# Optimization experiments

Hardware: AMD Instinct MI355X
Metric: run time of the kernel (lower is better)

## Reference

```python
import jax, jax.numpy as jnp
import numpy as np

DIM = 1024
N_HEADS = 16
HEAD_DIM = DIM // N_HEADS
B, T = 2, 2048


def setup_inputs() -> dict:
    key = jax.random.key(0)
    ks = jax.random.split(key, 5)
    x = jax.random.normal(ks[0], (B, T, DIM), dtype=jnp.float32)
    s = DIM ** -0.5
    Wq = jax.random.normal(ks[1], (DIM, DIM), dtype=jnp.float32) * s
    Wk = jax.random.normal(ks[2], (DIM, DIM), dtype=jnp.float32) * s
    Wv = jax.random.normal(ks[3], (DIM, DIM), dtype=jnp.float32) * s
    Wo = jax.random.normal(ks[4], (DIM, DIM), dtype=jnp.float32) * s
    # causal mask: 1 where attendable, 0 where masked (masked_fill on mask==0)
    mask = jnp.tril(jnp.ones((T, T), dtype=jnp.int32))[None, None, :, :]
    return {"x": x, "Wq": Wq, "Wk": Wk, "Wv": Wv, "Wo": Wo, "mask": mask}


def _rope_tables(seq_len, dim, dtype):
    inv_freq = 1.0 / (10000.0 ** (jnp.arange(0, dim, 2, dtype=jnp.float32) / dim))
    t = jnp.arange(seq_len, dtype=jnp.float32)
    freqs = jnp.outer(t, inv_freq)               # [T, dim/2]
    emb = jnp.concatenate([freqs, freqs], -1)    # [T, dim]
    return jnp.cos(emb).astype(dtype), jnp.sin(emb).astype(dtype)


def _rotate_half(t):
    h = t.shape[-1] // 2
    return jnp.concatenate([-t[..., h:], t[..., :h]], axis=-1)


def reference(x, Wq, Wk, Wv, Wo, mask):
    Bq, Tq, C = x.shape
    H, Dh = N_HEADS, C // N_HEADS
    q = (x @ Wq.T).reshape(Bq, Tq, H, Dh)
    k = (x @ Wk.T).reshape(Bq, Tq, H, Dh)
    v = (x @ Wv.T).reshape(Bq, Tq, H, Dh)
    cos, sin = _rope_tables(Tq, Dh, x.dtype)
    cos = cos[None, :, None, :]   # [1,T,1,Dh]
    sin = sin[None, :, None, :]
    q = q * cos + _rotate_half(q) * sin
    k = k * cos + _rotate_half(k) * sin
    scale = Dh ** -0.5
    # [B,H,T,T]
    attn = jnp.einsum('bqhd,bkhd->bhqk', q, k) * scale
    attn = jnp.where(mask == 0, jnp.float32(-jnp.inf).astype(attn.dtype), attn)
    attn = jax.nn.softmax(attn, axis=-1)
    out = jnp.einsum('bhqk,bkhd->bqhd', attn, v).reshape(Bq, Tq, C)
    return out @ Wo.T
```

## Files before the change

### kernel.cpp

```cpp
#include <hip/hip_runtime.h>
#include <stdint.h>


typedef float  f32x4  __attribute__((ext_vector_type(4)));
typedef float  f32x16 __attribute__((ext_vector_type(16)));
typedef __bf16 bf16x8 __attribute__((ext_vector_type(8)));
typedef unsigned int u32x2 __attribute__((ext_vector_type(2)));

#define GLDS16(gp, lp)                                                         \
  __builtin_amdgcn_global_load_lds(                                            \
      (const __attribute__((address_space(1))) void*)(gp),                     \
      (__attribute__((address_space(3))) void*)(lp), 16, 0, 0)

static __device__ __forceinline__ f32x4 zero4() {
  f32x4 z = {0.f, 0.f, 0.f, 0.f};
  return z;
}

static __device__ __forceinline__ bf16x8 cvt8(const float* __restrict__ p) {
  f32x4 u = *(const f32x4*)p;
  f32x4 v = *(const f32x4*)(p + 4);
  bf16x8 o;
#pragma unroll
  for (int j = 0; j < 4; ++j) o[j] = (__bf16)u[j];
#pragma unroll
  for (int j = 0; j < 4; ++j) o[4 + j] = (__bf16)v[j];
  return o;
}

__global__ __launch_bounds__(256) void prep(
    const float* __restrict__ x,
    const float* __restrict__ Wq, const float* __restrict__ Wk,
    const float* __restrict__ Wv, const float* __restrict__ Wo,
    __bf16* __restrict__ xb, __bf16* __restrict__ Wb)
{
  size_t g = ((size_t)blockIdx.x * 256 + threadIdx.x) * 8;
  if (g < (size_t)4194304) {
    *(bf16x8*)&xb[g] = cvt8(x + g);
  } else {
    size_t j = g - 4194304;
    int w = (int)(j >> 20);
    size_t off = j & 1048575;
    const float* src = (w == 0) ? Wq : (w == 1) ? Wk : (w == 2) ? Wv : Wo;
    *(bf16x8*)&Wb[(size_t)w * 1048576 + off] = cvt8(src + off);
  }
}

__global__ __launch_bounds__(256) void gemm_qkv(
    const __bf16* __restrict__ xb, const __bf16* __restrict__ Wb,
    __bf16* __restrict__ Qp, __bf16* __restrict__ Kp, __bf16* __restrict__ Vt)
{
  __shared__ __bf16 Smem[2][2 * 128 * 32];

  const int tid  = threadIdx.x;
  const int lane = tid & 63;
  const int wid  = tid >> 6;
  const int quad = lane >> 4;
  const int l16  = lane & 15;
  const int wm   = (wid >> 1) * 64;
  const int wn   = (wid & 1) * 64;

  const int lin = blockIdx.x;
  const int n0  = (lin & 7) * 128;
  const int r2  = lin >> 3;
  const int z   = r2 % 3;
  const int m0  = (r2 / 3) * 128;
  const __bf16* Bt = Wb + (size_t)z * 1048576;

  const int r0 = tid >> 2, c0 = tid & 3;
  const int r1 = r0 + 64;
  const int scx = (c0 ^ ((r0 >> 1) & 3)) * 8;
  const int fq  = (l16 >> 1) & 3;

  f32x4 acc[4][4];
  for (int i = 0; i < 4; ++i)
    for (int j = 0; j < 4; ++j) acc[i][j] = zero4();

#define QKV_STAGE(buf, k0)                                                     \
  do {                                                                         \
    __bf16* As_ = Smem[buf];                                                   \
    __bf16* Bs_ = Smem[buf] + 128 * 32;                                        \
    GLDS16(xb + (size_t)(m0 + r0) * 1024 + (k0) + scx, &As_[(size_t)tid * 8]); \
    GLDS16(xb + (size_t)(m0 + r1) * 1024 + (k0) + scx,                         \
           &As_[(size_t)(tid + 256) * 8]);                                     \
    GLDS16(Bt + (size_t)(n0 + r0) * 1024 + (k0) + scx, &Bs_[(size_t)tid * 8]); \
    GLDS16(Bt + (size_t)(n0 + r1) * 1024 + (k0) + scx,                         \
           &Bs_[(size_t)(tid + 256) * 8]);                                     \
  } while (0)

  QKV_STAGE(0, 0);
  __syncthreads();

  for (int k = 0; k < 32; ++k) {
    const int cur = k & 1;
    if (k < 31) QKV_STAGE(cur ^ 1, (k + 1) * 32);

    const __bf16* As = Smem[cur];
    const __bf16* Bs = Smem[cur] + 128 * 32;
    bf16x8 af[4], bfr[4];
#pragma unroll
    for (int i = 0; i < 4; ++i)
      af[i] = *(const bf16x8*)
          &As[(wm + i * 16 + l16) * 32 + ((quad ^ fq) * 8)];
#pragma unroll
    for (int i = 0; i < 4; ++i)
      bfr[i] = *(const bf16x8*)
          &Bs[(wn + i * 16 + l16) * 32 + ((quad ^ fq) * 8)];
    __builtin_amdgcn_s_setprio(1);
#pragma unroll
    for (int mt = 0; mt < 4; ++mt)
#pragma unroll
      for (int nt = 0; nt < 4; ++nt)
        acc[mt][nt] = __builtin_amdgcn_mfma_f32_16x16x32_bf16(
            af[mt], bfr[nt], acc[mt][nt], 0, 0, 0);
    __builtin_amdgcn_s_setprio(0);

    __syncthreads();
  }
#undef QKV_STAGE

  const int h = (n0 + wn) >> 6;
  __bf16* es = &Smem[0][wid * 1152];
  const int rl = lane >> 3, ch = lane & 7;

  if (z < 2) {
    const float c0f = -13.287712379549449f / 32.0f;
    const float f0 = exp2f((float)l16 * c0f);
    const float f1 = exp2f((float)(16 + l16) * c0f);
    const float SC = (z == 0) ? 0.125f * 1.44269504088896340736f : 1.0f;
    for (int mt = 0; mt < 4; ++mt)
      for (int r = 0; r < 4; ++r) {
        int gm = m0 + wm + mt * 16 + 4 * quad + r;
        float tt = (float)(gm & 2047);
        for (int nt = 0; nt < 2; ++nt) {
          float ang = tt * (nt ? f1 : f0);
          float cv = __cosf(ang) * SC, sv = __sinf(ang) * SC;
          float lo = acc[mt][nt][r], hi = acc[mt][nt + 2][r];
          acc[mt][nt][r]     = lo * cv - hi * sv;
          acc[mt][nt + 2][r] = hi * cv + lo * sv;
        }
      }
    __bf16* dst = (z == 0) ? Qp : Kp;
    for (int mt = 0; mt < 4; ++mt) {
      for (int nt = 0; nt < 4; ++nt)
        for (int r = 0; r < 4; ++r)
          es[(4 * quad + r) * 72 + nt * 16 + l16] = (__bf16)acc[mt][nt][r];
      size_t g0 = (size_t)(m0 + wm + mt * 16 + rl) * 1024 + n0 + wn + ch * 8;
      *(bf16x8*)&dst[g0]            = *(const bf16x8*)&es[rl * 72 + ch * 8];
      *(bf16x8*)&dst[g0 + 8 * 1024] = *(const bf16x8*)&es[(rl + 8) * 72 + ch * 8];
    }
  } else {
    const int b = m0 >> 11;
    const size_t hb = (size_t)(b * 16 + h) * 64;
    const int tt = (m0 + wm) & 2047;
    for (int nt = 0; nt < 4; ++nt) {
      for (int mt = 0; mt < 4; ++mt)
        for (int r = 0; r < 4; ++r)
          es[l16 * 72 + mt * 16 + 4 * quad + r] = (__bf16)acc[mt][nt][r];
      size_t g0 = (hb + nt * 16 + rl) * 2048 + tt + ch * 8;
      *(bf16x8*)&Vt[g0]                     = *(const bf16x8*)&es[rl * 72 + ch * 8];
      *(bf16x8*)&Vt[g0 + (size_t)8 * 2048]  = *(const bf16x8*)&es[(rl + 8) * 72 + ch * 8];
    }
  }
}

__global__ __launch_bounds__(256) void attn_fwd(
    __bf16* QA, const __bf16* __restrict__ Kp,
    const __bf16* __restrict__ Vt)
{
  __shared__ __bf16 Ks[2][64 * 64];
  __shared__ __bf16 Vs[2][64 * 64];

  const int tid  = threadIdx.x;
  const int lane = tid & 63, wid = tid >> 6;
  const int hl = lane >> 5, lq = lane & 31, lq7 = lq & 7;
  const int qh = wid & 1, kh = wid >> 1;

  const int L  = blockIdx.x;
  const int j  = L >> 3;
  const int qb = 31 - (j >> 2);
  const int bh = (L & 7) * 4 + (j & 3);
  const int b = bh >> 4, h = bh & 15;
  const int q0 = qb * 64;

  const size_t rowb = (size_t)b * 2048;
  const __bf16* Vb = Vt + (size_t)bh * 64 * 2048;

  const int srow = lane >> 3;
  const int scol = ((lane & 7) ^ srow) * 8;
  const int ck0 = wid * 2, ck1 = wid * 2 + 1;

  const int iql = qh * 32 + lq;

  bf16x8 qa[4];
#pragma unroll
  for (int ks = 0; ks < 4; ++ks)
    qa[ks] = *(const bf16x8*)
        &QA[(rowb + q0 + iql) * 1024 + h * 64 + ks * 16 + hl * 8];

  f32x16 oacc[2];
#pragma unroll
  for (int dt = 0; dt < 2; ++dt)
#pragma unroll
    for (int r = 0; r < 16; ++r) oacc[dt][r] = 0.f;
  float l_i = 0.f;

  const int kcmax = qb;

  GLDS16(Kp + (rowb + ck0 * 8 + srow) * 1024 + h * 64 + scol, &Ks[0][ck0 * 512]);
  GLDS16(Kp + (rowb + ck1 * 8 + srow) * 1024 + h * 64 + scol, &Ks[0][ck1 * 512]);
  GLDS16(Vb + (size_t)(ck0 * 8 + srow) * 2048 + scol, &Vs[0][ck0 * 512]);
  GLDS16(Vb + (size_t)(ck1 * 8 + srow) * 2048 + scol, &Vs[0][ck1 * 512]);
  __syncthreads();

  for (int kc = 0; kc <= kcmax; ++kc) {
    const int c = kc & 1;
    if (kc < kcmax) {
      const int t0 = (kc + 1) * 64;
      GLDS16(Kp + (rowb + t0 + ck0 * 8 + srow) * 1024 + h * 64 + scol,
             &Ks[c ^ 1][ck0 * 512]);
      GLDS16(Kp + (rowb + t0 + ck1 * 8 + srow) * 1024 + h * 64 + scol,
             &Ks[c ^ 1][ck1 * 512]);
      GLDS16(Vb + (size_t)(ck0 * 8 + srow) * 2048 + t0 + scol,
             &Vs[c ^ 1][ck0 * 512]);
      GLDS16(Vb + (size_t)(ck1 * 8 + srow) * 2048 + t0 + scol,
             &Vs[c ^ 1][ck1 * 512]);
    }

    const __bf16* Ksb = Ks[c];
    const __bf16* Vsb = Vs[c];

    f32x16 sacc;
#pragma unroll
    for (int r = 0; r < 16; ++r) sacc[r] = -16.f;
    __builtin_amdgcn_s_setprio(1);
#pragma unroll
    for (int ks = 0; ks < 4; ++ks) {
      bf16x8 kf = *(const bf16x8*)
          &Ksb[(kh * 32 + lq) * 64 + (((2 * ks + hl) ^ lq7) * 8)];
      sacc = __builtin_amdgcn_mfma_f32_32x32x16_bf16(kf, qa[ks], sacc, 0, 0, 0);
    }
    __builtin_amdgcn_s_setprio(0);

    const bool diag = (kc == kcmax);
    float p[16];
    float rsum = 0.f;
#pragma unroll
    for (int r = 0; r < 16; ++r) {
      float s = sacc[r];
      if (diag) {
        int kp = kh * 32 + (r & 3) + 8 * (r >> 2) + 4 * hl;
        if (kp > iql) s = -1e30f;
      }
      p[r] = __builtin_amdgcn_exp2f(s);
      rsum += p[r];
    }
    rsum += __shfl_xor(rsum, 32, 64);
    l_i += rsum;

    unsigned int cpk[8];
#pragma unroll
    for (int i = 0; i < 8; ++i)
      asm("v_cvt_pk_bf16_f32 %0, %1, %2"
          : "=v"(cpk[i]) : "v"(p[2 * i]), "v"(p[2 * i + 1]));
    bf16x8 pb[2];
#pragma unroll
    for (int k2 = 0; k2 < 2; ++k2) {
      unsigned int a0 = cpk[4 * k2 + 0], b0 = cpk[4 * k2 + 2];
      unsigned int a1 = cpk[4 * k2 + 1], b1 = cpk[4 * k2 + 3];
      asm("v_permlane32_swap_b32 %0, %1" : "+v"(a0), "+v"(b0));
      asm("v_permlane32_swap_b32 %0, %1" : "+v"(a1), "+v"(b1));
      union { unsigned int w[4]; bf16x8 v; } u;
      u.w[0] = a0; u.w[1] = a1; u.w[2] = b0; u.w[3] = b1;
      pb[k2] = u.v;
    }

    __builtin_amdgcn_s_setprio(1);
#pragma unroll
    for (int dt = 0; dt < 2; ++dt)
#pragma unroll
      for (int k2 = 0; k2 < 2; ++k2) {
        bf16x8 vf = *(const bf16x8*)
            &Vsb[(dt * 32 + lq) * 64 + (((4 * kh + 2 * k2 + hl) ^ lq7) * 8)];
        oacc[dt] = __builtin_amdgcn_mfma_f32_32x32x16_bf16(
            vf, pb[k2], oacc[dt], 0, 0, 0);
      }
    __builtin_amdgcn_s_setprio(0);

    __syncthreads();
  }

  float* Osf = (float*)&Ks[0][0];
  float* Lsf = (float*)&Vs[0][0];
  if (kh == 1) {
#pragma unroll
    for (int dt = 0; dt < 2; ++dt) {
      float* base = &Osf[((qh * 2 + dt) * 64 + lane) * 16];
#pragma unroll
      for (int g = 0; g < 4; ++g) {
        f32x4 w = {oacc[dt][4 * g], oacc[dt][4 * g + 1],
                   oacc[dt][4 * g + 2], oacc[dt][4 * g + 3]};
        *(f32x4*)&base[4 * g] = w;
      }
    }
    Lsf[qh * 64 + lane] = l_i;
  }
  __syncthreads();
  if (kh == 0) {
#pragma unroll
    for (int dt = 0; dt < 2; ++dt) {
      const float* base = &Osf[((qh * 2 + dt) * 64 + lane) * 16];
#pragma unroll
      for (int g = 0; g < 4; ++g) {
        f32x4 w = *(const f32x4*)&base[4 * g];
#pragma unroll
        for (int e = 0; e < 4; ++e) oacc[dt][4 * g + e] += w[e];
      }
    }
    float inv = 1.0f / (l_i + Lsf[qh * 64 + lane]);
#pragma unroll
    for (int dt = 0; dt < 2; ++dt)
#pragma unroll
      for (int g = 0; g < 4; ++g) {
        float a = oacc[dt][4 * g]     * inv, bb = oacc[dt][4 * g + 1] * inv;
        float cc = oacc[dt][4 * g + 2] * inv, dd = oacc[dt][4 * g + 3] * inv;
        unsigned int w0, w1;
        asm("v_cvt_pk_bf16_f32 %0, %1, %2" : "=v"(w0) : "v"(a), "v"(bb));
        asm("v_cvt_pk_bf16_f32 %0, %1, %2" : "=v"(w1) : "v"(cc), "v"(dd));
        u32x2 wv = {w0, w1};
        *(u32x2*)&QA[(rowb + q0 + iql) * 1024 + h * 64 + dt * 32 + 8 * g + 4 * hl] = wv;
      }
  }
}

__global__ __launch_bounds__(256) void gemm_out(
    const __bf16* __restrict__ AO, const __bf16* __restrict__ Wob,
    float* __restrict__ Of)
{
  __shared__ __bf16 Smem[2][192 * 32];

  const int tid  = threadIdx.x;
  const int lane = tid & 63;
  const int wid  = tid >> 6;
  const int quad = lane >> 4;
  const int l16  = lane & 15;
  const int wm   = (wid >> 1) * 32;
  const int wn   = (wid & 1) * 64;

  const int lin = blockIdx.x;
  const int n0  = (lin & 7) * 128;
  const int m0  = (lin >> 3) * 64;

  const int r0 = tid >> 2, c0 = tid & 3;
  const int scx = (c0 ^ ((r0 >> 1) & 3)) * 8;
  const int fq  = (l16 >> 1) & 3;

  f32x4 acc[2][4];
  for (int i = 0; i < 2; ++i)
    for (int j = 0; j < 4; ++j) acc[i][j] = zero4();

#define OUT_STAGE(buf, k0)                                                     \
  do {                                                                         \
    __bf16* As_ = Smem[buf];                                                   \
    __bf16* Bs_ = Smem[buf] + 64 * 32;                                         \
    GLDS16(AO  + (size_t)(m0 + r0) * 1024 + (k0) + scx, &As_[(size_t)tid * 8]);\
    GLDS16(Wob + (size_t)(n0 + r0) * 1024 + (k0) + scx, &Bs_[(size_t)tid * 8]);\
    GLDS16(Wob + (size_t)(n0 + 64 + r0) * 1024 + (k0) + scx,                   \
           &Bs_[(size_t)(tid + 256) * 8]);                                     \
  } while (0)

  OUT_STAGE(0, 0);
  __syncthreads();

  for (int k = 0; k < 32; ++k) {
    const int cur = k & 1;
    if (k < 31) OUT_STAGE(cur ^ 1, (k + 1) * 32);

    const __bf16* As = Smem[cur];
    const __bf16* Bs = Smem[cur] + 64 * 32;
    bf16x8 af[2], bfr[4];
#pragma unroll
    for (int i = 0; i < 2; ++i)
      af[i] = *(const bf16x8*)
          &As[(wm + i * 16 + l16) * 32 + ((quad ^ fq) * 8)];
#pragma unroll
    for (int i = 0; i < 4; ++i)
      bfr[i] = *(const bf16x8*)
          &Bs[(wn + i * 16 + l16) * 32 + ((quad ^ fq) * 8)];
    __builtin_amdgcn_s_setprio(1);
#pragma unroll
    for (int mt = 0; mt < 2; ++mt)
#pragma unroll
      for (int nt = 0; nt < 4; ++nt)
        acc[mt][nt] = __builtin_amdgcn_mfma_f32_16x16x32_bf16(
            af[mt], bfr[nt], acc[mt][nt], 0, 0, 0);
    __builtin_amdgcn_s_setprio(0);

    __syncthreads();
  }
#undef OUT_STAGE

  float* es = (float*)&Smem[0][0] + wid * 1088;
  const int rl = lane >> 4, ch = lane & 15;
  for (int mt = 0; mt < 2; ++mt) {
    for (int nt = 0; nt < 4; ++nt)
      for (int r = 0; r < 4; ++r)
        es[(4 * quad + r) * 68 + nt * 16 + l16] = acc[mt][nt][r];
    size_t g0 = (size_t)(m0 + wm + mt * 16 + rl) * 1024 + n0 + wn + ch * 4;
    *(f32x4*)&Of[g0]             = *(const f32x4*)&es[rl * 68 + ch * 4];
    *(f32x4*)&Of[g0 + 4 * 1024]  = *(const f32x4*)&es[(rl + 4) * 68 + ch * 4];
    *(f32x4*)&Of[g0 + 8 * 1024]  = *(const f32x4*)&es[(rl + 8) * 68 + ch * 4];
    *(f32x4*)&Of[g0 + 12 * 1024] = *(const f32x4*)&es[(rl + 12) * 68 + ch * 4];
  }
}

__global__ __launch_bounds__(256) void copy_bf16x8(
    const __bf16* __restrict__ src, __bf16* __restrict__ dst)
{
  size_t i = ((size_t)blockIdx.x * 256 + threadIdx.x) * 8;
  *(bf16x8*)&dst[i] = *(const bf16x8*)&src[i];
}

extern "C" void kernel_launch(void* const* d_in, const int* in_sizes, int n_in,
                              void* d_out, int out_size, void* d_ws, size_t ws_size,
                              hipStream_t stream) {
  const float* x  = (const float*)d_in[0];
  const float* Wq = (const float*)d_in[1];
  const float* Wk = (const float*)d_in[2];
  const float* Wv = (const float*)d_in[3];
  const float* Wo = (const float*)d_in[4];
  float* out = (float*)d_out;

  const size_t NELT = (size_t)4194304;
  __bf16* Qp = (__bf16*)d_ws;
  __bf16* Kp = Qp + NELT;
  __bf16* Vt = Kp + NELT;
  __bf16* xb = (__bf16*)d_out;
  __bf16* Wb = xb + NELT;

  prep<<<dim3(4096), 256, 0, stream>>>(x, Wq, Wk, Wv, Wo, xb, Wb);
  gemm_qkv<<<dim3(768), 256, 0, stream>>>(xb, Wb, Qp, Kp, Vt);
  attn_fwd<<<dim3(1024), 256, 0, stream>>>(Qp, Kp, Vt);
  copy_bf16x8<<<dim3(512), 256, 0, stream>>>(Wb + 3 * NELT / 4, Kp);
  gemm_out<<<dim3(512), 256, 0, stream>>>(Qp, Kp, out);
}
```

Before: 185.3 us.

## Triple-buffer GEMM prefetch and write bf16 Wo directly to workspace

Both the QKV and output GEMMs move from double to triple-buffered LDS staging. Fine-grained vmcnt waits and raw s_barrier let global-to-LDS loads run two stages ahead. The prep kernel now writes the converted Wo into a separate workspace region, which removes the extra copy kernel launched before the output GEMM. The cost is more LDS per block, which may reduce occupancy, and 2 MB more workspace.

```diff
diff --git a/kernel.cpp b/kernel.cpp
--- a/kernel.cpp
+++ b/kernel.cpp
@@ -32,7 +32,8 @@
     const float* __restrict__ x,
     const float* __restrict__ Wq, const float* __restrict__ Wk,
     const float* __restrict__ Wv, const float* __restrict__ Wo,
-    __bf16* __restrict__ xb, __bf16* __restrict__ Wb)
+    __bf16* __restrict__ xb, __bf16* __restrict__ Wb,
+    __bf16* __restrict__ Wos)
 {
   size_t g = ((size_t)blockIdx.x * 256 + threadIdx.x) * 8;
   if (g < (size_t)4194304) {
@@ -41,8 +42,12 @@
     size_t j = g - 4194304;
     int w = (int)(j >> 20);
     size_t off = j & 1048575;
-    const float* src = (w == 0) ? Wq : (w == 1) ? Wk : (w == 2) ? Wv : Wo;
-    *(bf16x8*)&Wb[(size_t)w * 1048576 + off] = cvt8(src + off);
+    if (w == 3) {
+      *(bf16x8*)&Wos[off] = cvt8(Wo + off);
+    } else {
+      const float* src = (w == 0) ? Wq : (w == 1) ? Wk : Wv;
+      *(bf16x8*)&Wb[(size_t)w * 1048576 + off] = cvt8(src + off);
+    }
   }
 }
 
@@ -50,7 +55,7 @@
     const __bf16* __restrict__ xb, const __bf16* __restrict__ Wb,
     __bf16* __restrict__ Qp, __bf16* __restrict__ Kp, __bf16* __restrict__ Vt)
 {
-  __shared__ __bf16 Smem[2][2 * 128 * 32];
+  __shared__ __bf16 Smem[3][2 * 128 * 32];
 
   const int tid  = threadIdx.x;
   const int lane = tid & 63;
@@ -89,11 +94,15 @@
   } while (0)
 
   QKV_STAGE(0, 0);
-  __syncthreads();
+  QKV_STAGE(1, 32);
+  asm volatile("s_waitcnt vmcnt(4)" ::: "memory");
+  __builtin_amdgcn_sched_barrier(0);
+  __builtin_amdgcn_s_barrier();
+  __builtin_amdgcn_sched_barrier(0);
 
   for (int k = 0; k < 32; ++k) {
-    const int cur = k & 1;
-    if (k < 31) QKV_STAGE(cur ^ 1, (k + 1) * 32);
+    const int cur = k % 3;
+    if (k + 2 < 32) QKV_STAGE((k + 2) % 3, (k + 2) * 32);
 
     const __bf16* As = Smem[cur];
     const __bf16* Bs = Smem[cur] + 128 * 32;
@@ -115,9 +124,19 @@
             af[mt], bfr[nt], acc[mt][nt], 0, 0, 0);
     __builtin_amdgcn_s_setprio(0);
 
-    __syncthreads();
+    if (k < 31) {
+      if (k < 30)
+        asm volatile("s_waitcnt vmcnt(4)" ::: "memory");
+      else
+        asm volatile("s_waitcnt vmcnt(0)" ::: "memory");
+      __builtin_amdgcn_sched_barrier(0);
+      __builtin_amdgcn_s_barrier();
+      __builtin_amdgcn_sched_barrier(0);
+    }
   }
 #undef QKV_STAGE
+
+  __syncthreads();
 
   const int h = (n0 + wn) >> 6;
   __bf16* es = &Smem[0][wid * 1152];
@@ -337,7 +356,7 @@
     const __bf16* __restrict__ AO, const __bf16* __restrict__ Wob,
     float* __restrict__ Of)
 {
-  __shared__ __bf16 Smem[2][192 * 32];
+  __shared__ __bf16 Smem[3][192 * 32];
 
   const int tid  = threadIdx.x;
   const int lane = tid & 63;
@@ -370,11 +389,15 @@
   } while (0)
 
   OUT_STAGE(0, 0);
-  __syncthreads();
+  OUT_STAGE(1, 32);
+  asm volatile("s_waitcnt vmcnt(3)" ::: "memory");
+  __builtin_amdgcn_sched_barrier(0);
+  __builtin_amdgcn_s_barrier();
+  __builtin_amdgcn_sched_barrier(0);
 
   for (int k = 0; k < 32; ++k) {
-    const int cur = k & 1;
-    if (k < 31) OUT_STAGE(cur ^ 1, (k + 1) * 32);
+    const int cur = k % 3;
+    if (k + 2 < 32) OUT_STAGE((k + 2) % 3, (k + 2) * 32);
 
     const __bf16* As = Smem[cur];
     const __bf16* Bs = Smem[cur] + 64 * 32;
@@ -396,9 +419,19 @@
             af[mt], bfr[nt], acc[mt][nt], 0, 0, 0);
     __builtin_amdgcn_s_setprio(0);
 
-    __syncthreads();
+    if (k < 31) {
+      if (k < 30)
+        asm volatile("s_waitcnt vmcnt(3)" ::: "memory");
+      else
+        asm volatile("s_waitcnt vmcnt(0)" ::: "memory");
+      __builtin_amdgcn_sched_barrier(0);
+      __builtin_amdgcn_s_barrier();
+      __builtin_amdgcn_sched_barrier(0);
+    }
   }
 #undef OUT_STAGE
+
+  __syncthreads();
 
   float* es = (float*)&Smem[0][0] + wid * 1088;
   const int rl = lane >> 4, ch = lane & 15;
@@ -414,13 +447,6 @@
   }
 }
 
-__global__ __launch_bounds__(256) void copy_bf16x8(
-    const __bf16* __restrict__ src, __bf16* __restrict__ dst)
-{
-  size_t i = ((size_t)blockIdx.x * 256 + threadIdx.x) * 8;
-  *(bf16x8*)&dst[i] = *(const bf16x8*)&src[i];
-}
-
 extern "C" void kernel_launch(void* const* d_in, const int* in_sizes, int n_in,
                               void* d_out, int out_size, void* d_ws, size_t ws_size,
                               hipStream_t stream) {
@@ -432,15 +458,15 @@
   float* out = (float*)d_out;
 
   const size_t NELT = (size_t)4194304;
-  __bf16* Qp = (__bf16*)d_ws;
-  __bf16* Kp = Qp + NELT;
-  __bf16* Vt = Kp + NELT;
-  __bf16* xb = (__bf16*)d_out;
-  __bf16* Wb = xb + NELT;
-
-  prep<<<dim3(4096), 256, 0, stream>>>(x, Wq, Wk, Wv, Wo, xb, Wb);
+  __bf16* Qp  = (__bf16*)d_ws;
+  __bf16* Kp  = Qp + NELT;
+  __bf16* Vt  = Kp + NELT;
+  __bf16* Wos = Vt + NELT;
+  __bf16* xb  = (__bf16*)d_out;
+  __bf16* Wb  = xb + NELT;
+
+  prep<<<dim3(4096), 256, 0, stream>>>(x, Wq, Wk, Wv, Wo, xb, Wb, Wos);
   gemm_qkv<<<dim3(768), 256, 0, stream>>>(xb, Wb, Qp, Kp, Vt);
   attn_fwd<<<dim3(1024), 256, 0, stream>>>(Qp, Kp, Vt);
-  copy_bf16x8<<<dim3(512), 256, 0, stream>>>(Wb + 3 * NELT / 4, Kp);
-  gemm_out<<<dim3(512), 256, 0, stream>>>(Qp, Kp, out);
-}
+  gemm_out<<<dim3(512), 256, 0, stream>>>(Qp, Wos, out);
+}
```

Result: no change. 185.8 us (+0.3%).
